# Optimization experiments

Measured on AMD Instinct MI355X. Metric: run time of the kernel, lower is better.

## Reference

```python
import jax, jax.numpy as jnp
import numpy as np

N_GRAPH = 100000
N_CAND = 1000
N_EDGES = 3200000
F_IN = 32


def _param(k, shape):
    return jax.random.normal(k, shape, dtype=jnp.float32) * 0.1


def setup_inputs() -> dict:
    key = jax.random.key(0)
    ks = jax.random.split(key, 20)
    inp = {
        "x": jax.random.normal(ks[0], (N_GRAPH, F_IN), dtype=jnp.float32),
        "candidate_set": jax.random.normal(ks[1], (N_CAND, F_IN), dtype=jnp.float32),
        "edge_index": jax.random.randint(ks[2], (2, N_EDGES), 0, N_GRAPH, dtype=jnp.int32),
        # GCN stack 32 -> 16 -> 24 -> 32
        "W1": _param(ks[3], (F_IN, 16)), "b1": jnp.zeros((16,), jnp.float32),
        "W2": _param(ks[4], (16, 24)),   "b2": jnp.zeros((24,), jnp.float32),
        "W3": _param(ks[5], (24, 32)),   "b3": jnp.zeros((32,), jnp.float32),
        # start-node MLP: 32 -> 16 -> 1
        "Ws1": _param(ks[6], (32, 16)), "bs1": jnp.zeros((16,), jnp.float32),
        "Ws2": _param(ks[7], (16, 1)),  "bs2": jnp.zeros((1,), jnp.float32),
        # end-node MLP: 32 -> 24 -> 1
        "We1": _param(ks[8], (32, 24)), "be1": jnp.zeros((24,), jnp.float32),
        "We2": _param(ks[9], (24, 1)),  "be2": jnp.zeros((1,), jnp.float32),
    }
    return inp


def _relu6(v):
    return jnp.clip(v, 0.0, 6.0)


def _gcn(h, row, col, dinv, W, b, N):
    # PyG GCNConv: h @ W, then D^-1/2 (A+I) D^-1/2 aggregation, then + bias
    h = h @ W
    norm = (dinv[row] * dinv[col])[:, None]
    return jax.ops.segment_sum(h[row] * norm, col, num_segments=N) + b


def reference(x, candidate_set, edge_index, W1, b1, W2, b2, W3, b3,
              Ws1, bs1, Ws2, bs2, We1, be1, We2, be2):
    n_graph = x.shape[0]
    h = jnp.concatenate([x, candidate_set], axis=0)  # [N, F_IN]
    N = h.shape[0]
    sl = jnp.arange(N, dtype=edge_index.dtype)
    row = jnp.concatenate([edge_index[0], sl])  # self-loops appended
    col = jnp.concatenate([edge_index[1], sl])
    deg = jax.ops.segment_sum(jnp.ones(row.shape[0], h.dtype), col, num_segments=N)
    dinv = 1.0 / jnp.sqrt(deg)  # deg >= 1 thanks to self-loops

    for W, b in ((W1, b1), (W2, b2), (W3, b3)):
        h = _gcn(h, row, col, dinv, W, b, N)  # [N, 32] at the end

    # start-node head: softmax over nodes (dim 0)
    start_probs = jax.nn.softmax(_relu6(h @ Ws1 + bs1) @ Ws2 + bs2, axis=0)  # [N,1]
    mask = jnp.ones_like(start_probs).at[n_graph:].set(0.0)  # zero out candidates
    start_probs = start_probs * mask
    start_probs = jnp.where(start_probs == 0.0, 1e-10, start_probs)
    start_probs = start_probs.squeeze()  # [N]
    start_node = jax.random.categorical(jax.random.key(42), jnp.log(start_probs))

    # end-node head
    end_probs = jax.nn.softmax(_relu6(h @ We1 + be1) @ We2 + be2, axis=0)  # [N,1]
    end_probs = end_probs.at[start_node].set(0.0)
    end_probs = jnp.where(end_probs == 0.0, 1e-10, end_probs)
    end_probs = end_probs.squeeze()  # [N]
    end_node = jax.random.categorical(jax.random.key(43), jnp.log(end_probs))

    new_edge = jnp.stack([start_node, end_node]).astype(edge_index.dtype)[:, None]
    edge_index_new = jnp.concatenate([edge_index, new_edge], axis=1)
    return (h, start_probs, end_probs, start_node, end_node, edge_index_new)
```

## Files before the change

kernel.cpp:

```cpp
#include <hip/hip_runtime.h>
#include <math.h>

#define TPB 256
#define STPB 512
#define BNODES 256
#define EPB 8192
#define SENT (-1)
#define MAXBKT 512
#define STAGE_CAP 9472
#define PMS 3200

typedef _Float16 h8 __attribute__((ext_vector_type(8)));
typedef _Float16 hf;


__device__ __forceinline__ float jax_gumbel(unsigned key, unsigned i) {
  unsigned x0 = 0u, x1 = i;
  unsigned ks0 = 0u, ks1 = key, ks2 = key ^ 0x1BD11BDAu;
  x0 += ks0; x1 += ks1;
#define TFR(r) { x0 += x1; x1 = (x1 << (r)) | (x1 >> (32 - (r))); x1 ^= x0; }
  TFR(13) TFR(15) TFR(26) TFR(6)
  x0 += ks1; x1 += ks2 + 1u;
  TFR(17) TFR(29) TFR(16) TFR(24)
  x0 += ks2; x1 += ks0 + 2u;
  TFR(13) TFR(15) TFR(26) TFR(6)
  x0 += ks0; x1 += ks1 + 3u;
  TFR(17) TFR(29) TFR(16) TFR(24)
  x0 += ks1; x1 += ks2 + 4u;
  TFR(13) TFR(15) TFR(26) TFR(6)
  x0 += ks2; x1 += ks0 + 5u;
#undef TFR
  unsigned bits = x0 ^ x1;
  float f = __uint_as_float((bits >> 9) | 0x3f800000u) - 1.0f;
  float u = (f == 0.0f) ? 1.17549435e-38f : f;
  return -logf(-logf(u));
}

__global__ void prep_k(const float* __restrict__ W2, const float* __restrict__ W3,
                       const float* __restrict__ b1, const float* __restrict__ b2,
                       float* __restrict__ W23, float* __restrict__ bvA, float* __restrict__ bvB,
                       int* __restrict__ breal, int nbkt) {
  int t = threadIdx.x;
  for (int i = t; i < nbkt; i += TPB) breal[i] = 0;
  for (int idx = t; idx < 512; idx += TPB) {
    int i = idx >> 5, j = idx & 31;
    float s = 0.f;
    for (int k = 0; k < 24; k++) s += W2[i * 24 + k] * W3[k * 32 + j];
    W23[idx] = s;
  }
  __syncthreads();
  if (t < 32) {
    float sA = 0.f;
    for (int i = 0; i < 16; i++) sA += b1[i] * W23[i * 32 + t];
    bvA[t] = sA;
    float sB = 0.f;
    for (int k = 0; k < 24; k++) sB += b2[k] * W3[k * 32 + t];
    bvB[t] = sB;
  }
}

__global__ void hist2_k(const int* __restrict__ col, int* __restrict__ breal,
                        int ne, int nbkt) {
  __shared__ int h[MAXBKT];
  int t = threadIdx.x;
  for (int i = t; i < nbkt; i += TPB) h[i] = 0;
  __syncthreads();
  int base = blockIdx.x * EPB;
#pragma unroll
  for (int k = 0; k < EPB / TPB; k++) {
    int idx = base + k * TPB + t;
    if (idx < ne) atomicAdd(&h[col[idx] >> 8], 1);
  }
  __syncthreads();
  for (int i = t; i < nbkt; i += TPB) if (h[i]) atomicAdd(&breal[i], h[i]);
}

__global__ void sbase_k(const int* __restrict__ breal, int* __restrict__ rbase,
                        int* __restrict__ base, int* __restrict__ cursor,
                        int nbkt, int nblk) {
  __shared__ int sr[TPB], sp[TPB];
  int t = threadIdx.x;
  int vr[2], vp[2]; int tr = 0, tp = 0;
#pragma unroll
  for (int k = 0; k < 2; k++) {
    int i = t * 2 + k; int R = 0, P = 0;
    if (i < nbkt) {
      R = breal[i];
      int mn = (nblk < R) ? nblk : R;
      P = (R + 3 * mn + 15) & ~15;
    }
    vr[k] = R; vp[k] = P; tr += R; tp += P;
  }
  sr[t] = tr; sp[t] = tp; __syncthreads();
  for (int off = 1; off < TPB; off <<= 1) {
    int ar = (t >= off) ? sr[t - off] : 0;
    int ap = (t >= off) ? sp[t - off] : 0;
    __syncthreads();
    sr[t] += ar; sp[t] += ap;
    __syncthreads();
  }
  int er = sr[t] - tr, ep = sp[t] - tp;
#pragma unroll
  for (int k = 0; k < 2; k++) {
    int i = t * 2 + k;
    if (i < nbkt) { rbase[i] = er; base[i] = ep; cursor[i] = ep; }
    er += vr[k]; ep += vp[k];
  }
}

__global__ void __launch_bounds__(STPB, 1)
scat_k(const int* __restrict__ row, const int* __restrict__ col,
       int* __restrict__ cursor, int* __restrict__ pairs,
       float* __restrict__ e0, float* __restrict__ e1,
       int ne, int nbkt) {
  __shared__ int sbase[MAXBKT], lofs[MAXBKT], lcur[MAXBKT], lsz[MAXBKT];
  __shared__ int ssc[STPB];
  __shared__ int stage[STAGE_CAP];
  int t = threadIdx.x;
  int b = blockIdx.x;
  for (int i = t; i < nbkt; i += STPB) lsz[i] = 0;
  __syncthreads();
  int base0 = b * EPB;
#pragma unroll
  for (int k = 0; k < EPB / STPB; k++) {
    int idx = base0 + k * STPB + t;
    if (idx < ne) atomicAdd(&lsz[col[idx] >> 8], 1);
  }
  __syncthreads();
  int L = (t < nbkt) ? lsz[t] : 0;
  int P = (L + 3) & ~3;
  ssc[t] = P; __syncthreads();
  for (int off = 1; off < STPB; off <<= 1) {
    int a = (t >= off) ? ssc[t - off] : 0;
    __syncthreads();
    ssc[t] += a;
    __syncthreads();
  }
  int excl = ssc[t] - P;
  if (t < nbkt) {
    lofs[t] = excl; lcur[t] = excl;
    if (L) sbase[t] = atomicAdd(&cursor[t], P);
  }
  __syncthreads();
#pragma unroll
  for (int k = 0; k < EPB / STPB; k++) {
    int idx = base0 + k * STPB + t;
    if (idx < ne) {
      int c = col[idx];
      int r = row[idx];
      int p = atomicAdd(&lcur[c >> 8], 1);
      stage[p] = (r << 8) | (c & 255);
      e0[idx] = (float)r;
      e1[idx] = (float)c;
    }
  }
  __syncthreads();
  for (int i = t; i < nbkt; i += STPB) {
    int en = lofs[i] + lsz[i], pe = lofs[i] + ((lsz[i] + 3) & ~3);
    for (int p = en; p < pe; p++) stage[p] = SENT;
  }
  __syncthreads();
  int4* gp = (int4*)pairs;
  const int4* sp = (const int4*)stage;
  for (int i = t; i < nbkt; i += STPB) {
    int Li = lsz[i]; if (!Li) continue;
    int gb = sbase[i] >> 2, lb = lofs[i] >> 2, m = ((Li + 3) & ~3) >> 2;
    for (int q = 0; q < m; q++) gp[gb + q] = sp[lb + q];
  }
}

__global__ void bbuild_k(const int* __restrict__ pairs, const int* __restrict__ base,
                         const int* __restrict__ cursor, const int* __restrict__ rbase,
                         int* __restrict__ rp, float* __restrict__ dinv,
                         int* __restrict__ csr, int n, int ne) {
  int bkt = blockIdx.x;
  int lo = bkt << 8;
  int t = threadIdx.x;
  int pstart = base[bkt];
  int pend   = cursor[bkt];
  int rbase_ = rbase[bkt];
  __shared__ int cnt[BNODES], sc[BNODES], pos[BNODES];
  cnt[t] = 0; __syncthreads();
  for (int p = pstart + t; p < pend; p += TPB) {
    int e = pairs[p];
    if (e >= 0) atomicAdd(&cnt[e & 255], 1);
  }
  __syncthreads();
  int own = cnt[t];
  sc[t] = own; __syncthreads();
  for (int off = 1; off < BNODES; off <<= 1) {
    int add = (t >= off) ? sc[t - off] : 0;
    __syncthreads();
    sc[t] += add;
    __syncthreads();
  }
  int excl = sc[t] - own;
  if (lo + t < n) {
    rp[lo + t] = rbase_ + excl;
    dinv[lo + t] = 1.0f / sqrtf((float)(own + 1));
  }
  pos[t] = rbase_ + excl;
  __syncthreads();
  for (int p = pstart + t; p < pend; p += TPB) {
    int e = pairs[p];
    if (e >= 0) {
      int q = atomicAdd(&pos[e & 255], 1);
      csr[q] = e >> 8;
    }
  }
  if (bkt == 0 && t == 0) rp[n] = ne;
}

__global__ void gemm16h_k(const float* __restrict__ A, const float* __restrict__ A2, int nsplit,
                          const float* __restrict__ W, const float* __restrict__ dinv,
                          hf* __restrict__ out, int n) {
  constexpr int FIN = 32, FOUT = 16, FP = 16;
  constexpr int NODES = TPB / FP;
  __shared__ float Ws[FIN * FOUT];
  __shared__ float Hs[NODES * (FIN + 1)];
  int t = threadIdx.x;
  int base = blockIdx.x * NODES;
  for (int i = t; i < FIN * FOUT; i += TPB) Ws[i] = W[i];
  for (int i = t; i < NODES * FIN; i += TPB) {
    int nl = i / FIN, k = i - nl * FIN;
    int g = base + nl;
    float v = 0.f;
    if (g < n) v = (g < nsplit) ? A[(size_t)g * FIN + k] : A2[(size_t)(g - nsplit) * FIN + k];
    Hs[nl * (FIN + 1) + k] = v;
  }
  __syncthreads();
  int nl = t / FP, j = t % FP;
  int g = base + nl;
  if (g < n) {
    float acc = 0.f;
#pragma unroll
    for (int k = 0; k < FIN; k++) acc += Hs[nl * (FIN + 1) + k] * Ws[k * FOUT + j];
    out[(size_t)g * FOUT + j] = (hf)(acc * dinv[g]);
  }
}

__global__ void agghs_k(const h8* __restrict__ ts, const int* __restrict__ csr,
                        const int* __restrict__ rp, const float* __restrict__ dinv,
                        const float* __restrict__ sin_, float* __restrict__ u_out,
                        float* __restrict__ us_out, h8* __restrict__ outv, int n) {
  int wave = blockIdx.x * (TPB / 64) + (threadIdx.x >> 6);
  int lane = threadIdx.x & 63;
  int j = lane & 1;
  int grp = (lane >> 1) & 3;
  int nl = lane >> 3;
  int c = wave * 8 + nl;
  bool valid = (c < n);
  float acc[8] = {0.f, 0.f, 0.f, 0.f, 0.f, 0.f, 0.f, 0.f};
  float accS = 0.f;
  if (valid) {
    int s = rp[c], e = rp[c + 1];
    int ch0 = s >> 2, ch1 = (e + 3) >> 2;
    int nch = ch1 - ch0;
    int k0 = ch0 + ((nch * grp) >> 2);
    int k1 = ch0 + ((nch * (grp + 1)) >> 2);
    for (int ch = k0; ch < k1; ch++) {
      int base = ch << 2;
      int4 e4 = *(const int4*)(csr + base);
      bool b0 = (base     >= s) & (base     < e);
      bool b1 = (base + 1 >= s) & (base + 1 < e);
      bool b2 = (base + 2 >= s) & (base + 2 < e);
      bool b3 = (base + 3 >= s) & (base + 3 < e);
      int r0 = b0 ? e4.x : 0;
      int r1 = b1 ? e4.y : 0;
      int r2 = b2 ? e4.z : 0;
      int r3 = b3 ? e4.w : 0;
      float m0 = b0 ? 1.f : 0.f, m1 = b1 ? 1.f : 0.f;
      float m2 = b2 ? 1.f : 0.f, m3 = b3 ? 1.f : 0.f;
      h8 v0 = ts[(r0 << 1) | j];
      h8 v1 = ts[(r1 << 1) | j];
      h8 v2 = ts[(r2 << 1) | j];
      h8 v3 = ts[(r3 << 1) | j];
      float sA = sin_[j ? r2 : r0];
      float sB = sin_[j ? r3 : r1];
      accS += sA * (j ? m2 : m0) + sB * (j ? m3 : m1);
#pragma unroll
      for (int k = 0; k < 8; k++)
        acc[k] += m0 * (float)v0[k] + m1 * (float)v1[k] + m2 * (float)v2[k] + m3 * (float)v3[k];
    }
  }
  accS += __shfl_xor(accS, 1, 64);
#pragma unroll
  for (int off = 2; off <= 4; off <<= 1) {
#pragma unroll
    for (int k = 0; k < 8; k++) acc[k] += __shfl_xor(acc[k], off, 64);
    accS += __shfl_xor(accS, off, 64);
  }
  if (valid && grp == 0) {
    h8 self = ts[(c << 1) | j];
    float d = dinv[c];
    float scl = d * d;
    h8 o;
#pragma unroll
    for (int k = 0; k < 8; k++) o[k] = (hf)(scl * (acc[k] + (float)self[k]));
    outv[(c << 1) | j] = o;
    if (j == 0) {
      float u = d * (accS + sin_[c]);
      u_out[c] = u;
      if (us_out) us_out[c] = u * d;
    }
  }
}

__global__ void agghch_k(const h8* __restrict__ ts, const int* __restrict__ csr,
                         const int* __restrict__ rp, const float* __restrict__ dinv,
                         const float* __restrict__ a1, const float* __restrict__ a2,
                         const float* __restrict__ W23, const float* __restrict__ bvA,
                         const float* __restrict__ bvB, const float* __restrict__ b3,
                         const float* __restrict__ Ws1, const float* __restrict__ bs1,
                         const float* __restrict__ ws2, const float* __restrict__ bs2,
                         const float* __restrict__ We1, const float* __restrict__ be1,
                         const float* __restrict__ we2, const float* __restrict__ be2,
                         float* __restrict__ out, float* __restrict__ slog,
                         float* __restrict__ elog, float* __restrict__ pm, int n) {
  __shared__ float Ws[512], vA[32], vB[32], vb[32];
  __shared__ float t3s[32][17];
  __shared__ float h3s[32][33];
  __shared__ float W1s[512], W2s[768], b1s[16], b2s[24], v1s[16], v2s[24], sb2[2];
  __shared__ float sm1[32], su1[32], sm2[32], su2[32];
  int t = threadIdx.x;
  for (int i = t; i < 512; i += TPB) { Ws[i] = W23[i]; W1s[i] = Ws1[i]; }
  for (int i = t; i < 768; i += TPB) W2s[i] = We1[i];
  if (t < 32) { vA[t] = bvA[t]; vB[t] = bvB[t]; vb[t] = b3[t]; }
  if (t < 16) { b1s[t] = bs1[t]; v1s[t] = ws2[t]; }
  if (t < 24) { b2s[t] = be1[t]; v2s[t] = we2[t]; }
  if (t == 0) { sb2[0] = bs2[0]; sb2[1] = be2[0]; }
  int wave = t >> 6;
  int lane = t & 63;
  int j = lane & 1;
  int grp = (lane >> 1) & 3;
  int nl = lane >> 3;
  int nlb = wave * 8 + nl;
  int c = blockIdx.x * 32 + nlb;
  bool valid = (c < n);
  float acc[8] = {0.f, 0.f, 0.f, 0.f, 0.f, 0.f, 0.f, 0.f};
  if (valid) {
    int s = rp[c], e = rp[c + 1];
    int ch0 = s >> 2, ch1 = (e + 3) >> 2;
    int nch = ch1 - ch0;
    int k0 = ch0 + ((nch * grp) >> 2);
    int k1 = ch0 + ((nch * (grp + 1)) >> 2);
    for (int ch = k0; ch < k1; ch++) {
      int base = ch << 2;
      int4 e4 = *(const int4*)(csr + base);
      bool b0 = (base     >= s) & (base     < e);
      bool b1 = (base + 1 >= s) & (base + 1 < e);
      bool b2 = (base + 2 >= s) & (base + 2 < e);
      bool b3b = (base + 3 >= s) & (base + 3 < e);
      int r0 = b0 ? e4.x : 0;
      int r1 = b1 ? e4.y : 0;
      int r2 = b2 ? e4.z : 0;
      int r3 = b3b ? e4.w : 0;
      float m0 = b0 ? 1.f : 0.f, m1 = b1 ? 1.f : 0.f;
      float m2 = b2 ? 1.f : 0.f, m3 = b3b ? 1.f : 0.f;
      h8 v0 = ts[(r0 << 1) | j];
      h8 v1 = ts[(r1 << 1) | j];
      h8 v2 = ts[(r2 << 1) | j];
      h8 v3 = ts[(r3 << 1) | j];
#pragma unroll
      for (int k = 0; k < 8; k++)
        acc[k] += m0 * (float)v0[k] + m1 * (float)v1[k] + m2 * (float)v2[k] + m3 * (float)v3[k];
    }
  }
#pragma unroll
  for (int off = 2; off <= 4; off <<= 1) {
#pragma unroll
    for (int k = 0; k < 8; k++) acc[k] += __shfl_xor(acc[k], off, 64);
  }
  if (valid && grp == 0) {
    h8 self = ts[(c << 1) | j];
    float d = dinv[c];
#pragma unroll
    for (int k = 0; k < 8; k++) t3s[nlb][j * 8 + k] = d * (acc[k] + (float)self[k]);
  }
  __syncthreads();
  int n2 = t >> 3, jb = t & 7;
  int g = blockIdx.x * 32 + n2;
  if (g < n) {
    float av = a1[g], bv = a2[g];
#pragma unroll
    for (int q = 0; q < 4; q++) {
      int j2 = jb + q * 8;
      float acc2 = 0.f;
#pragma unroll
      for (int k = 0; k < 16; k++) acc2 += t3s[n2][k] * Ws[k * 32 + j2];
      float hv = acc2 + bv * vA[j2] + av * vB[j2] + vb[j2];
      out[(size_t)g * 32 + j2] = hv;
      h3s[n2][j2] = hv;
    }
  }
  __syncthreads();
  float sP = 0.f, eP = 0.f;
  if (g < n) {
#pragma unroll
    for (int jj = 0; jj < 16; jj += 8) {
      int jh = jj + jb;
      float a = b1s[jh];
#pragma unroll
      for (int k = 0; k < 32; k++) a += h3s[n2][k] * W1s[k * 16 + jh];
      a = fminf(fmaxf(a, 0.f), 6.f);
      sP += a * v1s[jh];
    }
#pragma unroll
    for (int jj = 0; jj < 24; jj += 8) {
      int jh = jj + jb;
      float a = b2s[jh];
#pragma unroll
      for (int k = 0; k < 32; k++) a += h3s[n2][k] * W2s[k * 24 + jh];
      a = fminf(fmaxf(a, 0.f), 6.f);
      eP += a * v2s[jh];
    }
  }
#pragma unroll
  for (int off = 1; off <= 4; off <<= 1) {
    sP += __shfl_xor(sP, off, 64);
    eP += __shfl_xor(eP, off, 64);
  }
  if (jb == 0) {
    float s = -3.402823466e+38f, e2 = -3.402823466e+38f, w = 0.f;
    if (g < n) {
      s = sP + sb2[0]; e2 = eP + sb2[1]; w = 1.f;
      slog[g] = s; elog[g] = e2;
    }
    sm1[n2] = s;  su1[n2] = w;
    sm2[n2] = e2; su2[n2] = w;
  }
  __syncthreads();
  for (int st = 16; st > 0; st >>= 1) {
    if (t < st) {
      float M = fmaxf(sm1[t], sm1[t + st]);
      su1[t] = su1[t] * expf(sm1[t] - M) + su1[t + st] * expf(sm1[t + st] - M);
      sm1[t] = M;
      float M2 = fmaxf(sm2[t], sm2[t + st]);
      su2[t] = su2[t] * expf(sm2[t] - M2) + su2[t + st] * expf(sm2[t + st] - M2);
      sm2[t] = M2;
    }
    __syncthreads();
  }
  if (t == 0) {
    pm[blockIdx.x] = sm1[0]; pm[PMS + blockIdx.x] = su1[0];
    pm[2 * PMS + blockIdx.x] = sm2[0]; pm[3 * PMS + blockIdx.x] = su2[0];
  }
}

template <int HEAD>
__global__ void pargmax_k(const float* __restrict__ logit, const float* __restrict__ pm, int nb,
                          const float* __restrict__ sval, const int* __restrict__ sidx,
                          float* __restrict__ outp, unsigned key, int n, int ngraph,
                          float* __restrict__ pval, int* __restrict__ pidx,
                          float* __restrict__ dnode) {
  int t = threadIdx.x;
  __shared__ float smM[TPB], smS[TPB];
  __shared__ float sv0[TPB]; __shared__ int si0[TPB];
  const float* pmM = pm + (HEAD ? 2 * PMS : 0);
  const float* pmS = pm + (HEAD ? 3 * PMS : PMS);
  float m = -3.402823466e+38f, s0 = 0.f;
  for (int i = t; i < nb; i += TPB) {
    float bm = pmM[i], bs = pmS[i];
    float M = fmaxf(m, bm);
    s0 = s0 * expf(m - M) + bs * expf(bm - M); m = M;
  }
  smM[t] = m; smS[t] = s0; __syncthreads();
  for (int st = 128; st > 0; st >>= 1) {
    if (t < st) {
      float M = fmaxf(smM[t], smM[t + st]);
      smS[t] = smS[t] * expf(smM[t] - M) + smS[t + st] * expf(smM[t + st] - M);
      smM[t] = M;
    }
    __syncthreads();
  }
  float mx = smM[0], sm = smS[0];
  int ban = -1;
  if (HEAD) {
    sv0[t] = sval[t]; si0[t] = sidx[t]; __syncthreads();
    for (int st = 128; st > 0; st >>= 1) {
      if (t < st) {
        float v2 = sv0[t + st]; int i2 = si0[t + st];
        if (v2 > sv0[t] || (v2 == sv0[t] && i2 < si0[t])) { sv0[t] = v2; si0[t] = i2; }
      }
      __syncthreads();
    }
    ban = si0[0];
    if (blockIdx.x == 0 && t == 0) dnode[0] = (float)ban;
  }
  float bv = -3.402823466e+38f;
  int bi = 0x7fffffff;
  for (int i = blockIdx.x * TPB + t; i < n; i += gridDim.x * TPB) {
    float p = expf(logit[i] - mx) / sm;
    if (HEAD == 0) { if (i >= ngraph) p = 0.f; }
    else           { if (i == ban) p = 0.f; }
    if (p == 0.f) p = 1e-10f;
    outp[i] = p;
    float v = logf(p) + jax_gumbel(key, (unsigned)i);
    if (v > bv) { bv = v; bi = i; }
  }
  __shared__ float sv[TPB]; __shared__ int si[TPB];
  sv[t] = bv; si[t] = bi; __syncthreads();
  for (int st = 128; st > 0; st >>= 1) {
    if (t < st) {
      float v2 = sv[t + st]; int i2 = si[t + st];
      if (v2 > sv[t] || (v2 == sv[t] && i2 < si[t])) { sv[t] = v2; si[t] = i2; }
    }
    __syncthreads();
  }
  if (t == 0) { pval[blockIdx.x] = sv[0]; pidx[blockIdx.x] = si[0]; }
}

__global__ void argmax_fin_end_k(const float* pval, const int* pidx, int nb,
                                 const float* dstart, float* p_end, float* p_e0, float* p_e1) {
  int t = threadIdx.x;
  float bv = (t < nb) ? pval[t] : -3.402823466e+38f;
  int bi = (t < nb) ? pidx[t] : 0x7fffffff;
  __shared__ float sv[TPB]; __shared__ int si[TPB];
  sv[t] = bv; si[t] = bi; __syncthreads();
  for (int st = 128; st > 0; st >>= 1) {
    if (t < st) {
      float v2 = sv[t + st]; int i2 = si[t + st];
      if (v2 > sv[t] || (v2 == sv[t] && i2 < si[t])) { sv[t] = v2; si[t] = i2; }
    }
    __syncthreads();
  }
  if (t == 0) {
    int en = si[0];
    p_end[0] = (float)en;
    p_e0[0] = dstart[0];
    p_e1[0] = (float)en;
  }
}

extern "C" void kernel_launch(void* const* d_in, const int* in_sizes, int n_in,
                              void* d_out, int out_size, void* d_ws, size_t ws_size,
                              hipStream_t stream) {
  const float* x    = (const float*)d_in[0];
  const float* cand = (const float*)d_in[1];
  const int*   ei   = (const int*)d_in[2];
  const float* W1 = (const float*)d_in[3];  const float* b1  = (const float*)d_in[4];
  const float* W2 = (const float*)d_in[5];  const float* b2  = (const float*)d_in[6];
  const float* W3 = (const float*)d_in[7];  const float* b3  = (const float*)d_in[8];
  const float* Ws1= (const float*)d_in[9];  const float* bs1 = (const float*)d_in[10];
  const float* Ws2= (const float*)d_in[11]; const float* bs2 = (const float*)d_in[12];
  const float* We1= (const float*)d_in[13]; const float* be1 = (const float*)d_in[14];
  const float* We2= (const float*)d_in[15]; const float* be2 = (const float*)d_in[16];

  const int nG = in_sizes[0] / 32, nC = in_sizes[1] / 32;
  const int n  = nG + nC;
  const int ne = in_sizes[2] / 2;

  float* out = (float*)d_out;
  const size_t OFF1 = (size_t)n * 32;
  const size_t OFF2 = OFF1 + n;
  const size_t OFF3 = OFF2 + n;
  const size_t OFF4 = OFF3 + 1;
  const size_t OFF5 = OFF4 + 1;

  const int NBKT = (n + BNODES - 1) / BNODES;
  const int NBLK = (ne + EPB - 1) / EPB;

  float* wf = (float*)d_ws;
  int*   wi = (int*)d_ws;
  size_t NP = (((size_t)n + 2) + 63) & ~(size_t)63;
  size_t o = 0;
  int*   rp    = wi + o; o += NP;
  int*   breal = wi + o; o += 512;
  int*   rbase = wi + o; o += 512;
  int*   bbase = wi + o; o += 512;
  int*   bcur  = wi + o; o += 512;
  float* dinv  = wf + o; o += NP;
  float* a1v   = wf + o; o += NP;
  float* a1s   = wf + o; o += NP;
  float* a2v   = wf + o; o += NP;
  float* w23   = wf + o; o += 512;
  float* bvA   = wf + o; o += 64;
  float* bvB   = wf + o; o += 64;
  float* slogv = wf + o; o += NP;
  float* elogv = wf + o; o += NP;
  float* pmA   = wf + o; o += 4 * PMS;
  float* aval  = wf + o; o += 512;
  int*   aidx  = wi + o; o += 512;
  hf*    hh0   = (hf*)(wf + o); o += (size_t)n * 8 + 64;
  hf*    hh1   = (hf*)(wf + o); o += (size_t)n * 8 + 64;
  int*   csr   = wi + o; o += (size_t)ne + 64;
  int*   pairs = wi + o; o += (size_t)ne + 700000;

  const int* row = ei;
  const int* col = ei + ne;

  prep_k<<<1, TPB, 0, stream>>>(W2, W3, b1, b2, w23, bvA, bvB, breal, NBKT);
  hist2_k<<<NBLK, TPB, 0, stream>>>(col, breal, ne, NBKT);
  sbase_k<<<1, TPB, 0, stream>>>(breal, rbase, bbase, bcur, NBKT, NBLK);
  scat_k<<<NBLK, STPB, 0, stream>>>(row, col, bcur, pairs,
                                    out + OFF5, out + OFF5 + ne + 1, ne, NBKT);
  bbuild_k<<<NBKT, TPB, 0, stream>>>(pairs, bbase, bcur, rbase, rp, dinv, csr, n, ne);

  gemm16h_k<<<(n + 15) / 16, TPB, 0, stream>>>(x, cand, nG, W1, dinv, hh0, n);
  int gH = (n + 31) / 32;
  agghs_k<<<gH, TPB, 0, stream>>>((const h8*)hh0, csr, rp, dinv, dinv, a1v, a1s, (h8*)hh1, n);
  agghs_k<<<gH, TPB, 0, stream>>>((const h8*)hh1, csr, rp, dinv, a1s, a2v, nullptr, (h8*)hh0, n);
  agghch_k<<<gH, TPB, 0, stream>>>((const h8*)hh0, csr, rp, dinv, a1v, a2v,
                                   w23, bvA, bvB, b3,
                                   Ws1, bs1, Ws2, bs2, We1, be1, We2, be2,
                                   out, slogv, elogv, pmA, n);

  pargmax_k<0><<<256, TPB, 0, stream>>>(slogv, pmA, gH, nullptr, nullptr,
                                        out + OFF1, 42u, n, nG, aval, aidx, nullptr);

  pargmax_k<1><<<256, TPB, 0, stream>>>(elogv, pmA, gH, aval, aidx,
                                        out + OFF2, 43u, n, nG, aval + 256, aidx + 256,
                                        out + OFF3);
  argmax_fin_end_k<<<1, TPB, 0, stream>>>(aval + 256, aidx + 256, 256, out + OFF3,
                                          out + OFF4, out + OFF5 + ne, out + OFF5 + 2 * (size_t)ne + 1);
}
```

Measured before the change: 341.0 us.

## Interleave per-node scalar into half-precision feature rows for gather locality

The per-node scalar used in the first two aggregation passes (dinv for layer 1, u·d for layer 2) is now stored inside each node's fp16 feature row, padding it to 40 bytes. It used to live in a separate float array. Each random neighbour gather can then fetch the features and the scalar from one nearby memory region, avoiding a second scattered cache-line access. The cost is a larger feature buffer, 16-byte vector loads that are only 8-byte aligned, and some rows that straddle cache lines.

Measured after the change: 345.9 us. About the same (+1.5%).

```diff
diff --git a/kernel.cpp b/kernel.cpp
--- a/kernel.cpp
+++ b/kernel.cpp
@@ -235,14 +235,16 @@
     float acc = 0.f;
 #pragma unroll
     for (int k = 0; k < FIN; k++) acc += Hs[nl * (FIN + 1) + k] * Ws[k * FOUT + j];
-    out[(size_t)g * FOUT + j] = (hf)(acc * dinv[g]);
-  }
-}
-
-__global__ void agghs_k(const h8* __restrict__ ts, const int* __restrict__ csr,
+    float d = dinv[g];
+    out[(size_t)g * 20 + j] = (hf)(acc * d);
+    if (j == 0) ((float*)out)[(size_t)g * 10 + 8] = d;
+  }
+}
+
+template <int WS>
+__global__ void agghs_k(const hf* __restrict__ ts, const int* __restrict__ csr,
                         const int* __restrict__ rp, const float* __restrict__ dinv,
-                        const float* __restrict__ sin_, float* __restrict__ u_out,
-                        float* __restrict__ us_out, h8* __restrict__ outv, int n) {
+                        float* __restrict__ u_out, hf* __restrict__ outv, int n) {
   int wave = blockIdx.x * (TPB / 64) + (threadIdx.x >> 6);
   int lane = threadIdx.x & 63;
   int j = lane & 1;
@@ -250,6 +252,7 @@
   int nl = lane >> 3;
   int c = wave * 8 + nl;
   bool valid = (c < n);
+  const float* tsf = (const float*)ts;
   float acc[8] = {0.f, 0.f, 0.f, 0.f, 0.f, 0.f, 0.f, 0.f};
   float accS = 0.f;
   if (valid) {
@@ -271,12 +274,12 @@
       int r3 = b3 ? e4.w : 0;
       float m0 = b0 ? 1.f : 0.f, m1 = b1 ? 1.f : 0.f;
       float m2 = b2 ? 1.f : 0.f, m3 = b3 ? 1.f : 0.f;
-      h8 v0 = ts[(r0 << 1) | j];
-      h8 v1 = ts[(r1 << 1) | j];
-      h8 v2 = ts[(r2 << 1) | j];
-      h8 v3 = ts[(r3 << 1) | j];
-      float sA = sin_[j ? r2 : r0];
-      float sB = sin_[j ? r3 : r1];
+      h8 v0 = *(const h8*)(ts + (size_t)r0 * 20 + j * 8);
+      h8 v1 = *(const h8*)(ts + (size_t)r1 * 20 + j * 8);
+      h8 v2 = *(const h8*)(ts + (size_t)r2 * 20 + j * 8);
+      h8 v3 = *(const h8*)(ts + (size_t)r3 * 20 + j * 8);
+      float sA = tsf[(size_t)(j ? r2 : r0) * 10 + 8];
+      float sB = tsf[(size_t)(j ? r3 : r1) * 10 + 8];
       accS += sA * (j ? m2 : m0) + sB * (j ? m3 : m1);
 #pragma unroll
       for (int k = 0; k < 8; k++)
@@ -291,17 +294,17 @@
     accS += __shfl_xor(accS, off, 64);
   }
   if (valid && grp == 0) {
-    h8 self = ts[(c << 1) | j];
+    h8 self = *(const h8*)(ts + (size_t)c * 20 + j * 8);
     float d = dinv[c];
     float scl = d * d;
     h8 o;
 #pragma unroll
     for (int k = 0; k < 8; k++) o[k] = (hf)(scl * (acc[k] + (float)self[k]));
-    outv[(c << 1) | j] = o;
+    *(h8*)(outv + (size_t)c * WS + j * 8) = o;
     if (j == 0) {
-      float u = d * (accS + sin_[c]);
+      float u = d * (accS + tsf[(size_t)c * 10 + 8]);
       u_out[c] = u;
-      if (us_out) us_out[c] = u * d;
+      if (WS == 20) ((float*)outv)[(size_t)c * 10 + 8] = u * d;
     }
   }
 }
@@ -571,7 +574,6 @@
   int*   bcur  = wi + o; o += 512;
   float* dinv  = wf + o; o += NP;
   float* a1v   = wf + o; o += NP;
-  float* a1s   = wf + o; o += NP;
   float* a2v   = wf + o; o += NP;
   float* w23   = wf + o; o += 512;
   float* bvA   = wf + o; o += 64;
@@ -581,8 +583,10 @@
   float* pmA   = wf + o; o += 4 * PMS;
   float* aval  = wf + o; o += 512;
   int*   aidx  = wi + o; o += 512;
-  hf*    hh0   = (hf*)(wf + o); o += (size_t)n * 8 + 64;
-  hf*    hh1   = (hf*)(wf + o); o += (size_t)n * 8 + 64;
+  o = (o + 3) & ~(size_t)3;
+  hf*    hh0   = (hf*)(wf + o); o += (size_t)n * 10 + 16;
+  hf*    hh1   = (hf*)(wf + o); o += (size_t)n * 10 + 16;
+  o = (o + 3) & ~(size_t)3;
   int*   csr   = wi + o; o += (size_t)ne + 64;
   int*   pairs = wi + o; o += (size_t)ne + 700000;
 
@@ -598,8 +602,8 @@
 
   gemm16h_k<<<(n + 15) / 16, TPB, 0, stream>>>(x, cand, nG, W1, dinv, hh0, n);
   int gH = (n + 31) / 32;
-  agghs_k<<<gH, TPB, 0, stream>>>((const h8*)hh0, csr, rp, dinv, dinv, a1v, a1s, (h8*)hh1, n);
-  agghs_k<<<gH, TPB, 0, stream>>>((const h8*)hh1, csr, rp, dinv, a1s, a2v, nullptr, (h8*)hh0, n);
+  agghs_k<20><<<gH, TPB, 0, stream>>>(hh0, csr, rp, dinv, a1v, hh1, n);
+  agghs_k<16><<<gH, TPB, 0, stream>>>(hh1, csr, rp, dinv, a2v, hh0, n);
   agghch_k<<<gH, TPB, 0, stream>>>((const h8*)hh0, csr, rp, dinv, a1v, a2v,
                                    w23, bvA, bvB, b3,
                                    Ws1, bs1, Ws2, bs2, We1, be1, We2, be2,
```
